# Kernel optimization log

Hardware: AMD Instinct MI355X
Metric: run time of the kernel (lower is better)

Reference implementation:

```python
import jax, jax.numpy as jnp
import numpy as np

PROMPT_N = 10
TOKEN_INDICES = (2, 5)
THRESHOLD = 0.85
LAMBDA_RETAIN = 1.0
LAMBDA_ERASE = -1.0
LAMBDA_SELF_RETAIN = 1.0
LAMBDA_SELF_ERASE = -1.0


def _resize_bilinear(img, oh, ow):
    """torch F.interpolate(mode='bilinear', align_corners=False) for a 2D image."""
    H, W = img.shape
    dt = img.dtype
    ys = jnp.clip((jnp.arange(oh, dtype=dt) + 0.5) * (H / oh) - 0.5, 0.0, H - 1.0)
    xs = jnp.clip((jnp.arange(ow, dtype=dt) + 0.5) * (W / ow) - 0.5, 0.0, W - 1.0)
    y0 = jnp.floor(ys).astype(jnp.int32)
    x0 = jnp.floor(xs).astype(jnp.int32)
    y1 = jnp.minimum(y0 + 1, H - 1)
    x1 = jnp.minimum(x0 + 1, W - 1)
    wy = (ys - y0.astype(dt))[:, None]   # (oh,1)
    wx = (xs - x0.astype(dt))[None, :]   # (1,ow)
    top = img[y0][:, x0] * (1 - wx) + img[y0][:, x1] * wx  # (oh,ow)
    bot = img[y1][:, x0] * (1 - wx) + img[y1][:, x1] * wx
    return top * (1 - wy) + bot * wy


def _token_flags():
    idxs = jnp.arange(1, PROMPT_N - 1)                      # tokens iterated: 1..prompt_n-2
    tok = jnp.asarray(TOKEN_INDICES)
    is_tok = (idxs[:, None] == tok[None, :]).any(axis=1)    # (C,)
    return idxs, is_tok


def _calc_mask(attn):
    h, w, _ = attn.shape
    idxs, is_tok = _token_flags()
    cols = jnp.transpose(attn[:, :, 1:PROMPT_N - 1], (2, 0, 1))          # (C,h,w)
    scaled = 255.0 * cols / jnp.max(cols, axis=(1, 2), keepdims=True)
    up = jax.vmap(lambda im: _resize_bilinear(im, 256, 256))(scaled)     # (C,256,256)
    thr = jnp.where(is_tok, THRESHOLD, THRESHOLD + 0.1)[:, None, None]
    mx = jnp.max(up, axis=(1, 2), keepdims=True)
    binary = jnp.where(up >= mx * thr, 255.0, 0.0)
    mask = jax.vmap(lambda im: _resize_bilinear(im, h, w))(binary)       # (C,h,w)
    return mask


def setup_inputs() -> dict:
    key = jax.random.key(0)
    k1, k2, k3, k4 = jax.random.split(key, 4)
    h, w, seq = 64, 64, 77
    return {
        "attn": jax.random.uniform(k1, (h, w, seq), dtype=jnp.float32),
        "attn_erase": jax.random.uniform(k2, (h, w, seq), dtype=jnp.float32),
        "self_attn": jax.random.uniform(k3, (h, w, h * w), dtype=jnp.float32),
        "self_attn_erase": jax.random.uniform(k4, (h, w, h * w), dtype=jnp.float32),
    }


def reference(attn, attn_erase, self_attn, self_attn_erase):
    h, w, seq = attn.shape
    hw = h * w
    idxs, is_tok = _token_flags()

    mask = _calc_mask(attn)                                   # (C,h,w)

    # cross-attn retain / erase: per-token-column MSE (mean over hw pixels)
    a = attn.reshape(hw, seq)
    ae = attn_erase.reshape(hw, seq)
    per_tok = jnp.mean((a - ae) ** 2, axis=0)                 # (seq,)
    sel = per_tok[idxs]                                       # (C,)
    retain_loss = jnp.sum(jnp.where(is_tok, 0.0, sel))
    erase_loss = jnp.sum(jnp.where(is_tok, sel, 0.0))

    # self-attn losses: per-pixel-column MSE (mean over hw), gated by mask>0
    Lj = jnp.mean((self_attn - self_attn_erase) ** 2, axis=(0, 1))   # (hw,)
    gates = (mask.reshape(PROMPT_N - 2, hw) > 0).astype(attn.dtype)  # (C,hw)
    per_i = gates @ Lj                                               # (C,)
    self_retain_loss = jnp.sum(jnp.where(is_tok, 0.0, per_i))
    self_erase_loss = jnp.sum(jnp.where(is_tok, per_i, 0.0))

    return (LAMBDA_RETAIN * retain_loss
            + LAMBDA_ERASE * erase_loss
            + LAMBDA_SELF_RETAIN * self_retain_loss
            + LAMBDA_SELF_ERASE * self_erase_loss)
```

## Files before the change

kernel.cpp:

```cpp
#include <hip/hip_runtime.h>

#define HWPIX 4096
#define SEQ   77
#define NBLK_SELF 2048

typedef float f32x4 __attribute__((ext_vector_type(4)));

__device__ __forceinline__ void coord(int i, int& i0, int& i1, float& w) {
    float s = fminf(fmaxf(0.25f * (float)i - 0.375f, 0.0f), 63.0f);
    i0 = (int)s;
    i1 = min(i0 + 1, 63);
    w = s - (float)i0;
}

__global__ __launch_bounds__(256) void kmax(const float* __restrict__ attn,
                                            float* __restrict__ ws_maxpart) {
    __shared__ float tile[10 * 64];
    __shared__ float red[4];
    const int c = blockIdx.x >> 3;
    const int g = blockIdx.x & 7;
    const int tok = c + 1;
    const int t = threadIdx.x;
    const int ybase = 8 * g - 1;

    for (int idx = t; idx < 640; idx += 256) {
        int rr = idx >> 6, x = idx & 63;
        int y = min(max(ybase + rr, 0), 63);
        tile[idx] = attn[(y * 64 + x) * SEQ + tok];
    }
    __syncthreads();

    int x0, x1; float wx;
    coord(t, x0, x1, wx);
    float m = -1e30f;
    int cy0 = -99, cy1 = -99;
    float r0 = 0.f, r1 = 0.f;
    for (int i = 32 * g; i < 32 * g + 32; ++i) {
        int y0, y1; float wy;
        coord(i, y0, y1, wy);
        if (y0 != cy0 || y1 != cy1) {
            int l0 = y0 - ybase, l1 = y1 - ybase;
            if (y0 == cy1) r0 = r1;
            else r0 = tile[l0 * 64 + x0] * (1.f - wx) + tile[l0 * 64 + x1] * wx;
            if (y1 == y0) r1 = r0;
            else r1 = tile[l1 * 64 + x0] * (1.f - wx) + tile[l1 * 64 + x1] * wx;
            cy0 = y0; cy1 = y1;
        }
        m = fmaxf(m, r0 * (1.f - wy) + r1 * wy);
    }
    #pragma unroll
    for (int off = 1; off < 64; off <<= 1)
        m = fmaxf(m, __shfl_xor(m, off, 64));
    if ((t & 63) == 0) red[t >> 6] = m;
    __syncthreads();
    if (t == 0)
        ws_maxpart[blockIdx.x] = fmaxf(fmaxf(red[0], red[1]), fmaxf(red[2], red[3]));
}

__global__ __launch_bounds__(256) void kgates(const float* __restrict__ attn,
                                              const float* __restrict__ attn_e,
                                              const float* __restrict__ ws_maxpart,
                                              float* __restrict__ wj,
                                              float* __restrict__ ws_crosspart) {
    const int bid = blockIdx.x;
    const int t = threadIdx.x;
    if (bid < 16) {
        const int j = bid * 256 + t;
        const int y = j >> 6, x = j & 63;
        float acc = 0.f;
        #pragma unroll
        for (int c = 0; c < 8; ++c) {
            const int tok = c + 1;
            const bool is_tok = (tok == 2) || (tok == 5);
            float mx = ws_maxpart[c * 8];
            #pragma unroll
            for (int g = 1; g < 8; ++g) mx = fmaxf(mx, ws_maxpart[c * 8 + g]);
            const float lim = mx * (is_tok ? 0.85f : 0.95f);
            bool gate = false;
            #pragma unroll
            for (int di = 1; di <= 2; ++di) {
                int y0, y1; float wy;
                coord(4 * y + di, y0, y1, wy);
                #pragma unroll
                for (int dj = 1; dj <= 2; ++dj) {
                    int xa, xb; float wxv;
                    coord(4 * x + dj, xa, xb, wxv);
                    float v00 = attn[(y0 * 64 + xa) * SEQ + tok];
                    float v01 = attn[(y0 * 64 + xb) * SEQ + tok];
                    float v10 = attn[(y1 * 64 + xa) * SEQ + tok];
                    float v11 = attn[(y1 * 64 + xb) * SEQ + tok];
                    float top = v00 * (1.f - wxv) + v01 * wxv;
                    float bot = v10 * (1.f - wxv) + v11 * wxv;
                    float u = top * (1.f - wy) + bot * wy;
                    gate = gate || (u >= lim);
                }
            }
            if (gate) acc += is_tok ? -1.f : 1.f;
        }
        wj[j] = acc;
    } else {
        __shared__ float red[4];
        const int tok = bid - 16 + 1;
        const bool is_tok = (tok == 2) || (tok == 5);
        float sum = 0.f;
        #pragma unroll
        for (int kk = 0; kk < 16; ++kk) {
            int p = t + kk * 256;
            float d = attn[p * SEQ + tok] - attn_e[p * SEQ + tok];
            sum += d * d;
        }
        #pragma unroll
        for (int off = 1; off < 64; off <<= 1) sum += __shfl_xor(sum, off, 64);
        if ((t & 63) == 0) red[t >> 6] = sum;
        __syncthreads();
        if (t == 0)
            ws_crosspart[bid - 16] =
                (is_tok ? -1.f : 1.f) * (red[0] + red[1] + red[2] + red[3]);
    }
}

__global__ __launch_bounds__(256) void kself(const float* __restrict__ a,
                                             const float* __restrict__ b,
                                             const float* __restrict__ wj,
                                             float* __restrict__ ws_partial) {
    __shared__ float red[4];
    const int t = threadIdx.x;
    const float* a0 = a + (size_t)blockIdx.x * 8192;
    const float* b0 = b + (size_t)blockIdx.x * 8192;
    const float* a1 = a0 + 4096;
    const float* b1 = b0 + 4096;
    const unsigned vo0 = (unsigned)t * 16u;
    const unsigned vo1 = vo0 + 4096u;
    const unsigned vo2 = vo0 + 8192u;
    const unsigned vo3 = vo0 + 12288u;
    f32x4 w0, w1, w2, w3, xa0, xa1, xa2, xa3, yb0, yb1, yb2, yb3;
    f32x4 xc0, xc1, xc2, xc3, yd0, yd1, yd2, yd3;
    asm volatile(
        "global_load_dwordx4 %0, %12, %16\n\t"
        "global_load_dwordx4 %1, %13, %16\n\t"
        "global_load_dwordx4 %2, %14, %16\n\t"
        "global_load_dwordx4 %3, %15, %16\n\t"
        "global_load_dwordx4 %4, %12, %17 nt\n\t"
        "global_load_dwordx4 %5, %13, %17 nt\n\t"
        "global_load_dwordx4 %6, %14, %17 nt\n\t"
        "global_load_dwordx4 %7, %15, %17 nt\n\t"
        "global_load_dwordx4 %8, %12, %18 nt\n\t"
        "global_load_dwordx4 %9, %13, %18 nt\n\t"
        "global_load_dwordx4 %10, %14, %18 nt\n\t"
        "global_load_dwordx4 %11, %15, %18 nt"
        : "=&v"(w0), "=&v"(w1), "=&v"(w2), "=&v"(w3),
          "=&v"(xa0), "=&v"(xa1), "=&v"(xa2), "=&v"(xa3),
          "=&v"(yb0), "=&v"(yb1), "=&v"(yb2), "=&v"(yb3)
        : "v"(vo0), "v"(vo1), "v"(vo2), "v"(vo3),
          "s"(wj), "s"(a0), "s"(b0));
    asm volatile(
        "global_load_dwordx4 %0, %8, %12 nt\n\t"
        "global_load_dwordx4 %1, %9, %12 nt\n\t"
        "global_load_dwordx4 %2, %10, %12 nt\n\t"
        "global_load_dwordx4 %3, %11, %12 nt\n\t"
        "global_load_dwordx4 %4, %8, %13 nt\n\t"
        "global_load_dwordx4 %5, %9, %13 nt\n\t"
        "global_load_dwordx4 %6, %10, %13 nt\n\t"
        "global_load_dwordx4 %7, %11, %13 nt\n\t"
        "s_waitcnt vmcnt(8)"
        : "=&v"(xc0), "=&v"(xc1), "=&v"(xc2), "=&v"(xc3),
          "=&v"(yd0), "=&v"(yd1), "=&v"(yd2), "=&v"(yd3)
        : "v"(vo0), "v"(vo1), "v"(vo2), "v"(vo3),
          "s"(a1), "s"(b1));
    __builtin_amdgcn_sched_barrier(0);
    float sum = 0.f;
    {
        float d0 = xa0.x - yb0.x, d1 = xa0.y - yb0.y, d2 = xa0.z - yb0.z, d3 = xa0.w - yb0.w;
        sum += w0.x * d0 * d0 + w0.y * d1 * d1 + w0.z * d2 * d2 + w0.w * d3 * d3;
        d0 = xa1.x - yb1.x; d1 = xa1.y - yb1.y; d2 = xa1.z - yb1.z; d3 = xa1.w - yb1.w;
        sum += w1.x * d0 * d0 + w1.y * d1 * d1 + w1.z * d2 * d2 + w1.w * d3 * d3;
        d0 = xa2.x - yb2.x; d1 = xa2.y - yb2.y; d2 = xa2.z - yb2.z; d3 = xa2.w - yb2.w;
        sum += w2.x * d0 * d0 + w2.y * d1 * d1 + w2.z * d2 * d2 + w2.w * d3 * d3;
        d0 = xa3.x - yb3.x; d1 = xa3.y - yb3.y; d2 = xa3.z - yb3.z; d3 = xa3.w - yb3.w;
        sum += w3.x * d0 * d0 + w3.y * d1 * d1 + w3.z * d2 * d2 + w3.w * d3 * d3;
    }
    asm volatile("s_waitcnt vmcnt(0)" ::: "memory");
    __builtin_amdgcn_sched_barrier(0);
    {
        float d0 = xc0.x - yd0.x, d1 = xc0.y - yd0.y, d2 = xc0.z - yd0.z, d3 = xc0.w - yd0.w;
        sum += w0.x * d0 * d0 + w0.y * d1 * d1 + w0.z * d2 * d2 + w0.w * d3 * d3;
        d0 = xc1.x - yd1.x; d1 = xc1.y - yd1.y; d2 = xc1.z - yd1.z; d3 = xc1.w - yd1.w;
        sum += w1.x * d0 * d0 + w1.y * d1 * d1 + w1.z * d2 * d2 + w1.w * d3 * d3;
        d0 = xc2.x - yd2.x; d1 = xc2.y - yd2.y; d2 = xc2.z - yd2.z; d3 = xc2.w - yd2.w;
        sum += w2.x * d0 * d0 + w2.y * d1 * d1 + w2.z * d2 * d2 + w2.w * d3 * d3;
        d0 = xc3.x - yd3.x; d1 = xc3.y - yd3.y; d2 = xc3.z - yd3.z; d3 = xc3.w - yd3.w;
        sum += w3.x * d0 * d0 + w3.y * d1 * d1 + w3.z * d2 * d2 + w3.w * d3 * d3;
    }
    #pragma unroll
    for (int off = 1; off < 64; off <<= 1) sum += __shfl_xor(sum, off, 64);
    if ((t & 63) == 0) red[t >> 6] = sum;
    __syncthreads();
    if (t == 0)
        ws_partial[blockIdx.x] = red[0] + red[1] + red[2] + red[3];
}

__global__ __launch_bounds__(256) void kfin(const float* __restrict__ ws_partial,
                                            const float* __restrict__ ws_crosspart,
                                            float* __restrict__ out) {
    __shared__ float red[4];
    const int t = threadIdx.x;
    float sum = 0.f;
    #pragma unroll
    for (int k = 0; k < 8; ++k) sum += ws_partial[t + k * 256];
    #pragma unroll
    for (int off = 1; off < 64; off <<= 1) sum += __shfl_xor(sum, off, 64);
    if ((t & 63) == 0) red[t >> 6] = sum;
    __syncthreads();
    if (t == 0) {
        float tot = red[0] + red[1] + red[2] + red[3];
        #pragma unroll
        for (int k = 0; k < 8; ++k) tot += ws_crosspart[k];
        out[0] = tot * (1.0f / HWPIX);
    }
}

extern "C" void kernel_launch(void* const* d_in, const int* in_sizes, int n_in,
                              void* d_out, int out_size, void* d_ws, size_t ws_size,
                              hipStream_t stream) {
    const float* attn   = (const float*)d_in[0];
    const float* attn_e = (const float*)d_in[1];
    const float* sa     = (const float*)d_in[2];
    const float* sae    = (const float*)d_in[3];
    float* out = (float*)d_out;
    float* wj      = (float*)d_ws;
    float* ws_maxp = wj + HWPIX;
    float* ws_crop = wj + HWPIX + 64;
    float* ws_part = wj + 4352;

    kmax  <<<64,        256, 0, stream>>>(attn, ws_maxp);
    kgates<<<24,        256, 0, stream>>>(attn, attn_e, ws_maxp, wj, ws_crop);
    kself <<<NBLK_SELF, 256, 0, stream>>>(sa, sae, wj, ws_part);
    kfin  <<<1,         256, 0, stream>>>(ws_part, ws_crop, out);
}
```

Before: 38.44 us.

## Compact nonzero gate columns and gather only them in self-attention pass

Adds a single-block compaction kernel that builds a list of the column indices and weights whose gate weight is nonzero, plus their count. The self-attention kernel then gathers only those columns when the count is at most 512, and otherwise falls back to the original dense vectorized loads. This is meant to cut HBM traffic when the mask is sparse. It costs an extra launch and a serialized scan, and scattered scalar gathers may still touch most cache lines.

Result: slower. 44.05 us (+14.6%).

```diff
diff --git a/kernel.cpp b/kernel.cpp
--- a/kernel.cpp
+++ b/kernel.cpp
@@ -3,6 +3,7 @@
 #define HWPIX 4096
 #define SEQ   77
 #define NBLK_SELF 2048
+#define SPARSE_MAX 512
 
 typedef float f32x4 __attribute__((ext_vector_type(4)));
 
@@ -119,77 +120,130 @@
     }
 }
 
+__global__ __launch_bounds__(256) void kcompact(const float* __restrict__ wj,
+                                                int* __restrict__ idxlist,
+                                                float* __restrict__ wlist,
+                                                int* __restrict__ nnz_out) {
+    __shared__ int cnt[64];
+    __shared__ int scan[64];
+    const int t = threadIdx.x;
+    const int wid = t >> 6, lane = t & 63;
+    float wv[16];
+    int within[16];
+    unsigned predbits = 0;
+    #pragma unroll
+    for (int k = 0; k < 16; ++k) {
+        wv[k] = wj[k * 256 + t];
+        bool p = (wv[k] != 0.f);
+        unsigned long long m = __ballot(p);
+        if (p) predbits |= (1u << k);
+        within[k] = __popcll(m & ((1ull << lane) - 1ull));
+        if (lane == 0) cnt[k * 4 + wid] = __popcll(m);
+    }
+    __syncthreads();
+    if (t == 0) {
+        int s = 0;
+        for (int q = 0; q < 64; ++q) { scan[q] = s; s += cnt[q]; }
+        nnz_out[0] = s;
+    }
+    __syncthreads();
+    #pragma unroll
+    for (int k = 0; k < 16; ++k) {
+        if (predbits & (1u << k)) {
+            int pos = scan[k * 4 + wid] + within[k];
+            idxlist[pos] = k * 256 + t;
+            wlist[pos] = wv[k];
+        }
+    }
+}
+
 __global__ __launch_bounds__(256) void kself(const float* __restrict__ a,
                                              const float* __restrict__ b,
                                              const float* __restrict__ wj,
+                                             const int* __restrict__ idxlist,
+                                             const float* __restrict__ wlist,
+                                             const int* __restrict__ nnz_p,
                                              float* __restrict__ ws_partial) {
     __shared__ float red[4];
     const int t = threadIdx.x;
-    const float* a0 = a + (size_t)blockIdx.x * 8192;
-    const float* b0 = b + (size_t)blockIdx.x * 8192;
-    const float* a1 = a0 + 4096;
-    const float* b1 = b0 + 4096;
-    const unsigned vo0 = (unsigned)t * 16u;
-    const unsigned vo1 = vo0 + 4096u;
-    const unsigned vo2 = vo0 + 8192u;
-    const unsigned vo3 = vo0 + 12288u;
-    f32x4 w0, w1, w2, w3, xa0, xa1, xa2, xa3, yb0, yb1, yb2, yb3;
-    f32x4 xc0, xc1, xc2, xc3, yd0, yd1, yd2, yd3;
-    asm volatile(
-        "global_load_dwordx4 %0, %12, %16\n\t"
-        "global_load_dwordx4 %1, %13, %16\n\t"
-        "global_load_dwordx4 %2, %14, %16\n\t"
-        "global_load_dwordx4 %3, %15, %16\n\t"
-        "global_load_dwordx4 %4, %12, %17 nt\n\t"
-        "global_load_dwordx4 %5, %13, %17 nt\n\t"
-        "global_load_dwordx4 %6, %14, %17 nt\n\t"
-        "global_load_dwordx4 %7, %15, %17 nt\n\t"
-        "global_load_dwordx4 %8, %12, %18 nt\n\t"
-        "global_load_dwordx4 %9, %13, %18 nt\n\t"
-        "global_load_dwordx4 %10, %14, %18 nt\n\t"
-        "global_load_dwordx4 %11, %15, %18 nt"
-        : "=&v"(w0), "=&v"(w1), "=&v"(w2), "=&v"(w3),
-          "=&v"(xa0), "=&v"(xa1), "=&v"(xa2), "=&v"(xa3),
-          "=&v"(yb0), "=&v"(yb1), "=&v"(yb2), "=&v"(yb3)
-        : "v"(vo0), "v"(vo1), "v"(vo2), "v"(vo3),
-          "s"(wj), "s"(a0), "s"(b0));
-    asm volatile(
-        "global_load_dwordx4 %0, %8, %12 nt\n\t"
-        "global_load_dwordx4 %1, %9, %12 nt\n\t"
-        "global_load_dwordx4 %2, %10, %12 nt\n\t"
-        "global_load_dwordx4 %3, %11, %12 nt\n\t"
-        "global_load_dwordx4 %4, %8, %13 nt\n\t"
-        "global_load_dwordx4 %5, %9, %13 nt\n\t"
-        "global_load_dwordx4 %6, %10, %13 nt\n\t"
-        "global_load_dwordx4 %7, %11, %13 nt\n\t"
-        "s_waitcnt vmcnt(8)"
-        : "=&v"(xc0), "=&v"(xc1), "=&v"(xc2), "=&v"(xc3),
-          "=&v"(yd0), "=&v"(yd1), "=&v"(yd2), "=&v"(yd3)
-        : "v"(vo0), "v"(vo1), "v"(vo2), "v"(vo3),
-          "s"(a1), "s"(b1));
-    __builtin_amdgcn_sched_barrier(0);
+    const int nnz = nnz_p[0];
     float sum = 0.f;
-    {
-        float d0 = xa0.x - yb0.x, d1 = xa0.y - yb0.y, d2 = xa0.z - yb0.z, d3 = xa0.w - yb0.w;
-        sum += w0.x * d0 * d0 + w0.y * d1 * d1 + w0.z * d2 * d2 + w0.w * d3 * d3;
-        d0 = xa1.x - yb1.x; d1 = xa1.y - yb1.y; d2 = xa1.z - yb1.z; d3 = xa1.w - yb1.w;
-        sum += w1.x * d0 * d0 + w1.y * d1 * d1 + w1.z * d2 * d2 + w1.w * d3 * d3;
-        d0 = xa2.x - yb2.x; d1 = xa2.y - yb2.y; d2 = xa2.z - yb2.z; d3 = xa2.w - yb2.w;
-        sum += w2.x * d0 * d0 + w2.y * d1 * d1 + w2.z * d2 * d2 + w2.w * d3 * d3;
-        d0 = xa3.x - yb3.x; d1 = xa3.y - yb3.y; d2 = xa3.z - yb3.z; d3 = xa3.w - yb3.w;
-        sum += w3.x * d0 * d0 + w3.y * d1 * d1 + w3.z * d2 * d2 + w3.w * d3 * d3;
-    }
-    asm volatile("s_waitcnt vmcnt(0)" ::: "memory");
-    __builtin_amdgcn_sched_barrier(0);
-    {
-        float d0 = xc0.x - yd0.x, d1 = xc0.y - yd0.y, d2 = xc0.z - yd0.z, d3 = xc0.w - yd0.w;
-        sum += w0.x * d0 * d0 + w0.y * d1 * d1 + w0.z * d2 * d2 + w0.w * d3 * d3;
-        d0 = xc1.x - yd1.x; d1 = xc1.y - yd1.y; d2 = xc1.z - yd1.z; d3 = xc1.w - yd1.w;
-        sum += w1.x * d0 * d0 + w1.y * d1 * d1 + w1.z * d2 * d2 + w1.w * d3 * d3;
-        d0 = xc2.x - yd2.x; d1 = xc2.y - yd2.y; d2 = xc2.z - yd2.z; d3 = xc2.w - yd2.w;
-        sum += w2.x * d0 * d0 + w2.y * d1 * d1 + w2.z * d2 * d2 + w2.w * d3 * d3;
-        d0 = xc3.x - yd3.x; d1 = xc3.y - yd3.y; d2 = xc3.z - yd3.z; d3 = xc3.w - yd3.w;
-        sum += w3.x * d0 * d0 + w3.y * d1 * d1 + w3.z * d2 * d2 + w3.w * d3 * d3;
+    if (nnz <= SPARSE_MAX) {
+        const size_t r0 = (size_t)blockIdx.x * 8192;
+        const size_t r1 = r0 + 4096;
+        for (int i = t; i < nnz; i += 256) {
+            int j = idxlist[i];
+            float w = wlist[i];
+            float d0 = a[r0 + j] - b[r0 + j];
+            float d1 = a[r1 + j] - b[r1 + j];
+            sum += w * (d0 * d0 + d1 * d1);
+        }
+    } else {
+        const float* a0 = a + (size_t)blockIdx.x * 8192;
+        const float* b0 = b + (size_t)blockIdx.x * 8192;
+        const float* a1 = a0 + 4096;
+        const float* b1 = b0 + 4096;
+        const unsigned vo0 = (unsigned)t * 16u;
+        const unsigned vo1 = vo0 + 4096u;
+        const unsigned vo2 = vo0 + 8192u;
+        const unsigned vo3 = vo0 + 12288u;
+        f32x4 w0, w1, w2, w3, xa0, xa1, xa2, xa3, yb0, yb1, yb2, yb3;
+        f32x4 xc0, xc1, xc2, xc3, yd0, yd1, yd2, yd3;
+        asm volatile(
+            "global_load_dwordx4 %0, %12, %16\n\t"
+            "global_load_dwordx4 %1, %13, %16\n\t"
+            "global_load_dwordx4 %2, %14, %16\n\t"
+            "global_load_dwordx4 %3, %15, %16\n\t"
+            "global_load_dwordx4 %4, %12, %17 nt\n\t"
+            "global_load_dwordx4 %5, %13, %17 nt\n\t"
+            "global_load_dwordx4 %6, %14, %17 nt\n\t"
+            "global_load_dwordx4 %7, %15, %17 nt\n\t"
+            "global_load_dwordx4 %8, %12, %18 nt\n\t"
+            "global_load_dwordx4 %9, %13, %18 nt\n\t"
+            "global_load_dwordx4 %10, %14, %18 nt\n\t"
+            "global_load_dwordx4 %11, %15, %18 nt"
+            : "=&v"(w0), "=&v"(w1), "=&v"(w2), "=&v"(w3),
+              "=&v"(xa0), "=&v"(xa1), "=&v"(xa2), "=&v"(xa3),
+              "=&v"(yb0), "=&v"(yb1), "=&v"(yb2), "=&v"(yb3)
+            : "v"(vo0), "v"(vo1), "v"(vo2), "v"(vo3),
+              "s"(wj), "s"(a0), "s"(b0));
+        asm volatile(
+            "global_load_dwordx4 %0, %8, %12 nt\n\t"
+            "global_load_dwordx4 %1, %9, %12 nt\n\t"
+            "global_load_dwordx4 %2, %10, %12 nt\n\t"
+            "global_load_dwordx4 %3, %11, %12 nt\n\t"
+            "global_load_dwordx4 %4, %8, %13 nt\n\t"
+            "global_load_dwordx4 %5, %9, %13 nt\n\t"
+            "global_load_dwordx4 %6, %10, %13 nt\n\t"
+            "global_load_dwordx4 %7, %11, %13 nt\n\t"
+            "s_waitcnt vmcnt(8)"
+            : "=&v"(xc0), "=&v"(xc1), "=&v"(xc2), "=&v"(xc3),
+              "=&v"(yd0), "=&v"(yd1), "=&v"(yd2), "=&v"(yd3)
+            : "v"(vo0), "v"(vo1), "v"(vo2), "v"(vo3),
+              "s"(a1), "s"(b1));
+        __builtin_amdgcn_sched_barrier(0);
+        {
+            float d0 = xa0.x - yb0.x, d1 = xa0.y - yb0.y, d2 = xa0.z - yb0.z, d3 = xa0.w - yb0.w;
+            sum += w0.x * d0 * d0 + w0.y * d1 * d1 + w0.z * d2 * d2 + w0.w * d3 * d3;
+            d0 = xa1.x - yb1.x; d1 = xa1.y - yb1.y; d2 = xa1.z - yb1.z; d3 = xa1.w - yb1.w;
+            sum += w1.x * d0 * d0 + w1.y * d1 * d1 + w1.z * d2 * d2 + w1.w * d3 * d3;
+            d0 = xa2.x - yb2.x; d1 = xa2.y - yb2.y; d2 = xa2.z - yb2.z; d3 = xa2.w - yb2.w;
+            sum += w2.x * d0 * d0 + w2.y * d1 * d1 + w2.z * d2 * d2 + w2.w * d3 * d3;
+            d0 = xa3.x - yb3.x; d1 = xa3.y - yb3.y; d2 = xa3.z - yb3.z; d3 = xa3.w - yb3.w;
+            sum += w3.x * d0 * d0 + w3.y * d1 * d1 + w3.z * d2 * d2 + w3.w * d3 * d3;
+        }
+        asm volatile("s_waitcnt vmcnt(0)" ::: "memory");
+        __builtin_amdgcn_sched_barrier(0);
+        {
+            float d0 = xc0.x - yd0.x, d1 = xc0.y - yd0.y, d2 = xc0.z - yd0.z, d3 = xc0.w - yd0.w;
+            sum += w0.x * d0 * d0 + w0.y * d1 * d1 + w0.z * d2 * d2 + w0.w * d3 * d3;
+            d0 = xc1.x - yd1.x; d1 = xc1.y - yd1.y; d2 = xc1.z - yd1.z; d3 = xc1.w - yd1.w;
+            sum += w1.x * d0 * d0 + w1.y * d1 * d1 + w1.z * d2 * d2 + w1.w * d3 * d3;
+            d0 = xc2.x - yd2.x; d1 = xc2.y - yd2.y; d2 = xc2.z - yd2.z; d3 = xc2.w - yd2.w;
+            sum += w2.x * d0 * d0 + w2.y * d1 * d1 + w2.z * d2 * d2 + w2.w * d3 * d3;
+            d0 = xc3.x - yd3.x; d1 = xc3.y - yd3.y; d2 = xc3.z - yd3.z; d3 = xc3.w - yd3.w;
+            sum += w3.x * d0 * d0 + w3.y * d1 * d1 + w3.z * d2 * d2 + w3.w * d3 * d3;
+        }
     }
     #pragma unroll
     for (int off = 1; off < 64; off <<= 1) sum += __shfl_xor(sum, off, 64);
@@ -229,11 +283,15 @@
     float* out = (float*)d_out;
     float* wj      = (float*)d_ws;
     float* ws_maxp = wj + HWPIX;
-    float* ws_crop = wj + HWPIX + 64;
-    float* ws_part = wj + 4352;
-
-    kmax  <<<64,        256, 0, stream>>>(attn, ws_maxp);
-    kgates<<<24,        256, 0, stream>>>(attn, attn_e, ws_maxp, wj, ws_crop);
-    kself <<<NBLK_SELF, 256, 0, stream>>>(sa, sae, wj, ws_part);
-    kfin  <<<1,         256, 0, stream>>>(ws_part, ws_crop, out);
-}
+    float* ws_crop = wj + 4160;
+    int*   ws_nnz  = (int*)(wj + 4168);
+    int*   ws_idx  = (int*)(wj + 4224);
+    float* ws_wl   = wj + 8320;
+    float* ws_part = wj + 12416;
+
+    kmax    <<<64,        256, 0, stream>>>(attn, ws_maxp);
+    kgates  <<<24,        256, 0, stream>>>(attn, attn_e, ws_maxp, wj, ws_crop);
+    kcompact<<<1,         256, 0, stream>>>(wj, ws_idx, ws_wl, ws_nnz);
+    kself   <<<NBLK_SELF, 256, 0, stream>>>(sa, sae, wj, ws_idx, ws_wl, ws_nnz, ws_part);
+    kfin    <<<1,         256, 0, stream>>>(ws_part, ws_crop, out);
+}
```
